# Kernel optimization log

Measured on AMD Instinct MI355X. Metric: run time of the kernel, lower is better.

The kernel has to match this reference:

```python
import jax, jax.numpy as jnp
import numpy as np
import math

RADIUS = 1.0
PERCENTAGES = (0.004, 0.006, 0.008, 0.01, 0.012)
REPULSION_H = 0.0005


def pairwise_sqdist(a, b):
    # a: [..., M, 3], b: [..., N, 3] -> [..., M, N] squared euclidean distances
    d = (jnp.sum(a * a, -1)[..., :, None] + jnp.sum(b * b, -1)[..., None, :]
         - 2.0 * jnp.einsum('...md,...nd->...mn', a, b))
    return jnp.maximum(d, 0.0)


def fps_indices(pts, npoint):
    # furthest point sampling for one cloud; pts [N,3] -> [npoint] int32 (starts at index 0)
    N = pts.shape[0]
    def body(carry, _):
        mind, last = carry
        d = jnp.sum((pts - pts[last]) ** 2, axis=-1)
        mind = jnp.minimum(mind, d)
        nxt = jnp.argmax(mind).astype(jnp.int32)
        return (mind, nxt), nxt
    init = (jnp.full((N,), 1e10, pts.dtype), jnp.int32(0))
    _, idxs = jax.lax.scan(body, init, None, length=npoint - 1)
    return jnp.concatenate([jnp.zeros((1,), jnp.int32), idxs])


def ball_query(pcd, new_xyz, r, nsample):
    # pcd [B,N,3], new_xyz [B,S,3] -> idx [B,S,nsample] int32
    # first-found-in-order semantics, pad with first valid index (pn2 ball_query)
    B, N, _ = pcd.shape
    sqd = pairwise_sqdist(new_xyz, pcd)                 # [B,S,N]
    mask = sqd < (r * r)
    key = jnp.where(mask, jnp.arange(N, dtype=jnp.int32)[None, None, :], jnp.int32(N))
    order = jnp.sort(key, axis=-1)[..., :nsample]       # in-ball indices first, ascending
    first = order[..., :1]                              # query is in cloud -> always valid
    return jnp.where(order == N, first, order)


def uniform_loss(pcd, radius=RADIUS):
    B, N, _ = pcd.shape
    npoint = int(N * 0.05)
    fps_idx = jax.vmap(fps_indices, in_axes=(0, None))(pcd, npoint)       # [B,npoint]
    new_xyz = jax.vmap(lambda p, i: p[i])(pcd, fps_idx)                    # [B,npoint,3]
    loss = jnp.float32(0.0)
    for p in PERCENTAGES:
        nsample = int(N * p)
        r = math.sqrt(p * radius)
        disk_area = math.pi * (radius ** 2) / N
        expect_len = math.sqrt(disk_area)
        idx = ball_query(pcd, new_xyz, r, nsample)                         # [B,npoint,nsample]
        grouped = jax.vmap(lambda pc, i: pc[i])(pcd, idx)                  # [B,npoint,nsample,3]
        g = grouped.reshape(B * npoint, nsample, 3)
        sqd = pairwise_sqdist(g, g)                                        # [G,ns,ns]
        # KNN k=2: two smallest sqdists; index 1 is nearest non-self neighbor
        sq2 = -jax.lax.top_k(-sqd, 2)[0][..., 1]                           # [G,ns]
        dist = jnp.sqrt(sq2 + 1e-12)                                       # knn returns euclidean dist
        uniform_dist = jnp.abs(dist + 1e-8)
        u = jnp.mean(uniform_dist, axis=1)                                 # [G]
        u = (u - expect_len) ** 2 / (expect_len + 1e-8)
        loss = loss + jnp.mean(u) * ((p * 100.0) ** 2)
    return loss / len(PERCENTAGES)


def repulsion_loss(pcd, h=REPULSION_H):
    sqd = pairwise_sqdist(pcd, pcd)                                        # [B,N,N]
    # knn k=20 then slice [:, :, 1:5]; only 5 smallest needed (same sorted values)
    vals = -jax.lax.top_k(-sqd, 5)[0]                                      # 5 smallest sqdists, ascending
    d = vals[..., 1:5]                                                     # dist**2 == sqdist
    return jnp.mean(jnp.maximum(h - d, 0.0))


def setup_inputs() -> dict:
    key = jax.random.key(0)
    pcd = jax.random.normal(key, (8, 4096, 3), dtype=jnp.float32)
    return {"pcd": pcd}


def reference(pcd):
    return uniform_loss(pcd) + repulsion_loss(pcd)
```

## Files before the change

### kernel.cpp

```cpp
#include <hip/hip_runtime.h>
#include <cmath>
#include <cstdint>

#define NB 8
#define NPTS 4096
#define NPOINT 204
#define NCENT (NB * NPOINT)

typedef unsigned long long u64;

struct BallParams { float thr[5]; int ns[5]; float el; float denom; };
struct FinalParams { double w[5]; };

template<int CTRL, int RMASK>
__device__ __forceinline__ u64 dpp_u64max_step(u64 v) {
    const int lo = (int)(unsigned)v, hi = (int)(unsigned)(v >> 32);
    const int lo2 = __builtin_amdgcn_update_dpp(lo, lo, CTRL, RMASK, 0xF, false);
    const int hi2 = __builtin_amdgcn_update_dpp(hi, hi, CTRL, RMASK, 0xF, false);
    const u64 o = ((u64)(unsigned)hi2 << 32) | (unsigned)lo2;
    return o > v ? o : v;
}
__device__ __forceinline__ u64 wave_u64max63(u64 v) {
    v = dpp_u64max_step<0x111, 0xF>(v);
    v = dpp_u64max_step<0x112, 0xF>(v);
    v = dpp_u64max_step<0x114, 0xF>(v);
    v = dpp_u64max_step<0x118, 0xF>(v);
    v = dpp_u64max_step<0x142, 0xA>(v);
    v = dpp_u64max_step<0x143, 0xC>(v);
    return v;
}
__device__ __forceinline__ u64 u64max(u64 a, u64 b) { return a > b ? a : b; }

__global__ __launch_bounds__(512) void fused_fps_rep(const float* __restrict__ pcd,
                                                     int* __restrict__ fps,
                                                     double* __restrict__ part)
{
#pragma clang fp contract(off)
    __shared__ float4 spts[NPTS];
    __shared__ int fps_lds[NPOINT];
    __shared__ __align__(16) u64 exch[2][8];
    __shared__ double wsum[8];

    const int t = threadIdx.x;
    const int lane = t & 63, wv = t >> 6;

    if (blockIdx.x < NB) {
        const int b = blockIdx.x;
        const float* base = pcd + (size_t)b * NPTS * 3;

        for (int j = t; j < NPTS; j += 512)
            spts[j] = make_float4(base[3*j], base[3*j+1], base[3*j+2], 0.f);

        const int pbase = t * 8;
        float px[8], py[8], pz[8], md[8];
#pragma unroll
        for (int k = 0; k < 8; ++k) {
            px[k] = base[(pbase + k) * 3 + 0];
            py[k] = base[(pbase + k) * 3 + 1];
            pz[k] = base[(pbase + k) * 3 + 2];
            md[k] = 1e10f;
        }
        if (t == 0) fps_lds[0] = 0;
        __syncthreads();

        float lx = spts[0].x, ly = spts[0].y, lz = spts[0].z;

        for (int it = 1; it < NPOINT; ++it) {
            u64 c[8];
#pragma unroll
            for (int k = 0; k < 8; ++k) {
                const float dx = px[k] - lx, dy = py[k] - ly, dz = pz[k] - lz;
                float d = dx * dx + dy * dy;
                d = d + dz * dz;
                const float m = fminf(md[k], d);
                md[k] = m;
                c[k] = ((u64)(unsigned)__float_as_int(m) << 32)
                     | (unsigned)(4095 - (pbase + k));
            }
#pragma unroll
            for (int s = 4; s >= 1; s >>= 1)
#pragma unroll
                for (int i = 0; i < 8; ++i)
                    if (i < s) c[i] = u64max(c[i], c[i + s]);
            const u64 wmax = wave_u64max63(c[0]);

            if (lane == 63) exch[it & 1][wv] = wmax;
            __syncthreads();

            const ulonglong2* e = (const ulonglong2*)&exch[it & 1][0];
            const ulonglong2 E0 = e[0], E1 = e[1], E2 = e[2], E3 = e[3];
            u64 m01 = u64max(E0.x, E0.y), m23 = u64max(E1.x, E1.y);
            u64 m45 = u64max(E2.x, E2.y), m67 = u64max(E3.x, E3.y);
            const u64 m = u64max(u64max(m01, m23), u64max(m45, m67));
            const int bi = 4095 - (int)((unsigned)m & 0xFFFu);

            if (t == 0) fps_lds[it] = bi;
            const float4 cc = spts[bi];
            lx = cc.x; ly = cc.y; lz = cc.z;
        }
        __syncthreads();
        for (int j = t; j < NPOINT; j += 512) fps[b * NPOINT + j] = fps_lds[j];
    } else {
        const int bb = blockIdx.x - NB;
        const int batch = bb >> 6;
        const int chunk = bb & 63;
        const float* base = pcd + (size_t)batch * NPTS * 3;

        for (int j = t; j < NPTS; j += 512) {
            const float x = base[j * 3 + 0], y = base[j * 3 + 1], z = base[j * 3 + 2];
            const float qs = (x * x + y * y) + z * z;
            spts[j] = make_float4(x, y, z, qs);
        }
        __syncthreads();

        const float h = 0.0005f;
        double acc = 0.0;

        for (int ii = 0; ii < 8; ++ii) {
            const int i = (chunk << 6) + (wv << 3) + ii;
            const float4 C = spts[i];
            const float cx = C.x, cy = C.y, cz = C.z, cs = C.w;
            float s0 = 3e38f, s1 = 3e38f, s2 = 3e38f, s3 = 3e38f;
            for (int bj = 0; bj < NPTS; bj += 64) {
                const int j = bj + lane;
                const float4 o = spts[j];
                const float dot = (cx * o.x + cy * o.y) + cz * o.z;
                const float d = fmaxf((cs + o.w) - 2.0f * dot, 0.0f);
                const bool q = (d < h) && (j != i);
                unsigned long long bal = __ballot(q);
                while (bal) {
                    const int src = __ffsll((unsigned long long)bal) - 1;
                    bal &= bal - 1;
                    const float dv = __shfl(d, src);
                    if (dv < s0) { s3 = s2; s2 = s1; s1 = s0; s0 = dv; }
                    else if (dv < s1) { s3 = s2; s2 = s1; s1 = dv; }
                    else if (dv < s2) { s3 = s2; s2 = dv; }
                    else if (dv < s3) { s3 = dv; }
                }
            }
            if (lane == 0) {
                if (s0 < h) acc += (double)(h - s0);
                if (s1 < h) acc += (double)(h - s1);
                if (s2 < h) acc += (double)(h - s2);
                if (s3 < h) acc += (double)(h - s3);
            }
        }
        if (lane == 0) wsum[wv] = acc;
        __syncthreads();
        if (t == 0) {
            double s = 0.0;
            for (int w = 0; w < 8; ++w) s += wsum[w];
            part[bb] = s;
        }
    }
}

__global__ __launch_bounds__(256) void ball_kernel(const float* __restrict__ pcd,
                                                   const int* __restrict__ fps,
                                                   double* __restrict__ uvals,
                                                   BallParams P)
{
#pragma clang fp contract(off)
    __shared__ float sqs[NPTS];
    __shared__ int wlist[4][5][52];
    __shared__ float4 gpts[4][64];

    const int wave = threadIdx.x >> 6;
    const int lane = threadIdx.x & 63;
    const int c = blockIdx.x * 4 + wave;
    const int b = c / NPOINT;
    const int m = c % NPOINT;

    const float* base = pcd + (size_t)b * NPTS * 3;
    for (int j = threadIdx.x; j < NPTS; j += 256) {
        const float x = base[j * 3 + 0], y = base[j * 3 + 1], z = base[j * 3 + 2];
        sqs[j] = (x * x + y * y) + z * z;
    }
    __syncthreads();

    const int ci = fps[b * NPOINT + m];
    const float cx = base[ci * 3 + 0], cy = base[ci * 3 + 1], cz = base[ci * 3 + 2];
    const float cs = sqs[ci];

    const int ns0 = P.ns[0], ns1 = P.ns[1], ns2 = P.ns[2], ns3 = P.ns[3], ns4 = P.ns[4];
    int cnt[5] = {0, 0, 0, 0, 0};
    const u64 lmask = (1ull << lane) - 1ull;

    for (int bj = 0; bj < NPTS; bj += 64) {
        const int j = bj + lane;
        const float qx = base[j * 3 + 0], qy = base[j * 3 + 1], qz = base[j * 3 + 2];
        const float qs = sqs[j];
        const float dot = (cx * qx + cy * qy) + cz * qz;
        const float d = fmaxf((cs + qs) - 2.0f * dot, 0.0f);

        const u64 bal4 = __ballot(d < P.thr[4]);
        if (bal4) {
#pragma unroll
            for (int p = 0; p < 4; ++p) {
                const bool q = d < P.thr[p];
                const u64 bal = __ballot(q);
                if (q) {
                    const int pos = cnt[p] + __popcll(bal & lmask);
                    if (pos < P.ns[p]) wlist[wave][p][pos] = j;
                }
                cnt[p] += __popcll(bal);
            }
            if (d < P.thr[4]) {
                const int pos = cnt[4] + __popcll(bal4 & lmask);
                if (pos < ns4) wlist[wave][4][pos] = j;
            }
            cnt[4] += __popcll(bal4);
            if (cnt[0] >= ns0 && cnt[1] >= ns1 && cnt[2] >= ns2 &&
                cnt[3] >= ns3 && cnt[4] >= ns4) break;
        }
    }

#pragma unroll
    for (int p = 0; p < 5; ++p) {
        const int nsample = P.ns[p];
        const int m_in = (cnt[p] < nsample) ? cnt[p] : nsample;
        const int gidx = wlist[wave][p][(lane < m_in) ? lane : 0];
        const float gx = base[gidx * 3 + 0], gy = base[gidx * 3 + 1], gz = base[gidx * 3 + 2];
        const float gs = sqs[gidx];
        gpts[wave][lane] = make_float4(gx, gy, gz, gs);

        float m1 = 3.0e38f, m2 = 3.0e38f;
        for (int j = 0; j < nsample; ++j) {
            const float4 o = gpts[wave][j];
            const float dot = (gx * o.x + gy * o.y) + gz * o.z;
            const float d = fmaxf((gs + o.w) - 2.0f * dot, 0.0f);
            if (d < m1) { m2 = m1; m1 = d; }
            else if (d < m2) { m2 = d; }
        }
        float ud = (lane < nsample) ? fabsf(sqrtf(m2 + 1e-12f) + 1e-8f) : 0.0f;
        for (int off = 32; off; off >>= 1) ud += __shfl_xor(ud, off);
        if (lane == 0) {
            const float um   = ud / (float)nsample;
            const float diff = um - P.el;
            const float u    = (diff * diff) / P.denom;
            uvals[p * NCENT + c] = (double)u;
        }
    }
}

__global__ __launch_bounds__(256) void final_kernel(const double* __restrict__ uvals,
                                                    const double* __restrict__ part,
                                                    float* __restrict__ out,
                                                    FinalParams F)
{
    __shared__ double red[6][4];
    const int t = threadIdx.x;
    const int lane = t & 63, wv = t >> 6;

    double s[6] = {0.0, 0.0, 0.0, 0.0, 0.0, 0.0};
    for (int c = t; c < NCENT; c += 256) {
        s[0] += uvals[0 * NCENT + c];
        s[1] += uvals[1 * NCENT + c];
        s[2] += uvals[2 * NCENT + c];
        s[3] += uvals[3 * NCENT + c];
        s[4] += uvals[4 * NCENT + c];
    }
    for (int c = t; c < NB * 64; c += 256) s[5] += part[c];

    for (int off = 32; off; off >>= 1) {
#pragma unroll
        for (int p = 0; p < 6; ++p) s[p] += __shfl_xor(s[p], off);
    }
    if (lane == 0) {
#pragma unroll
        for (int p = 0; p < 6; ++p) red[p][wv] = s[p];
    }
    __syncthreads();
    if (t == 0) {
        double sums[6];
#pragma unroll
        for (int p = 0; p < 6; ++p)
            sums[p] = ((red[p][0] + red[p][1]) + red[p][2]) + red[p][3];
        double loss = 0.0;
        loss += (sums[0] / (double)NCENT) * F.w[0];
        loss += (sums[1] / (double)NCENT) * F.w[1];
        loss += (sums[2] / (double)NCENT) * F.w[2];
        loss += (sums[3] / (double)NCENT) * F.w[3];
        loss += (sums[4] / (double)NCENT) * F.w[4];
        loss /= 5.0;
        const double rep = sums[5] / (double)(NB * NPTS * 4);
        out[0] = (float)(loss + rep);
    }
}

extern "C" void kernel_launch(void* const* d_in, const int* in_sizes, int n_in,
                              void* d_out, int out_size, void* d_ws, size_t ws_size,
                              hipStream_t stream)
{
    const float* pcd = (const float*)d_in[0];
    float* out = (float*)d_out;

    int*    fps   = (int*)d_ws;
    double* uvals = (double*)((char*)d_ws + 8192);
    double* repp  = (double*)((char*)d_ws + 8192 + (size_t)5 * NCENT * 8);

    const double pv[5] = {0.004, 0.006, 0.008, 0.01, 0.012};
    const int    nsv[5] = {16, 24, 32, 40, 49};

    BallParams bp;
    FinalParams fp;
    for (int i = 0; i < 5; ++i) {
        const double r = sqrt(pv[i]);
        bp.thr[i] = (float)(r * r);
        bp.ns[i]  = nsv[i];
        const double w = pv[i] * 100.0;
        fp.w[i] = w * w;
    }
    const double el = sqrt(3.141592653589793 / 4096.0);
    bp.el    = (float)el;
    bp.denom = (float)(el + 1e-8);

    fused_fps_rep<<<NB + NB * 64, 512, 0, stream>>>(pcd, fps, repp);
    ball_kernel<<<NCENT / 4, 256, 0, stream>>>(pcd, fps, uvals, bp);
    final_kernel<<<1, 256, 0, stream>>>(uvals, repp, out, fp);
}
```

Measured before the change: 175.4 us.

## Split each ball query across four waves and drop shared sqnorm table

Each block now handles one centroid instead of four. Its four waves each scan a quarter of the point cloud, and the per-wave in-ball lists are merged in order through shared counts. The five radius groups are then spread across the waves for the nearest-neighbour step. The per-block 4096-entry squared-norm table is replaced by computing norms inline. This shortens the serial scan per centroid and removes the shared-memory preload, but gives up the early-exit break, so all points are always scanned.

```diff
diff --git a/kernel.cpp b/kernel.cpp
--- a/kernel.cpp
+++ b/kernel.cpp
@@ -161,35 +161,29 @@
                                                    BallParams P)
 {
 #pragma clang fp contract(off)
-    __shared__ float sqs[NPTS];
     __shared__ int wlist[4][5][52];
+    __shared__ int scnt[4][5];
     __shared__ float4 gpts[4][64];
 
     const int wave = threadIdx.x >> 6;
     const int lane = threadIdx.x & 63;
-    const int c = blockIdx.x * 4 + wave;
+    const int c = blockIdx.x;
     const int b = c / NPOINT;
     const int m = c % NPOINT;
 
     const float* base = pcd + (size_t)b * NPTS * 3;
-    for (int j = threadIdx.x; j < NPTS; j += 256) {
-        const float x = base[j * 3 + 0], y = base[j * 3 + 1], z = base[j * 3 + 2];
-        sqs[j] = (x * x + y * y) + z * z;
-    }
-    __syncthreads();
-
     const int ci = fps[b * NPOINT + m];
     const float cx = base[ci * 3 + 0], cy = base[ci * 3 + 1], cz = base[ci * 3 + 2];
-    const float cs = sqs[ci];
-
-    const int ns0 = P.ns[0], ns1 = P.ns[1], ns2 = P.ns[2], ns3 = P.ns[3], ns4 = P.ns[4];
+    const float cs = (cx * cx + cy * cy) + cz * cz;
+
     int cnt[5] = {0, 0, 0, 0, 0};
     const u64 lmask = (1ull << lane) - 1ull;
 
-    for (int bj = 0; bj < NPTS; bj += 64) {
-        const int j = bj + lane;
+    const int j0 = wave << 10;
+    for (int bj = 0; bj < 1024; bj += 64) {
+        const int j = j0 + bj + lane;
         const float qx = base[j * 3 + 0], qy = base[j * 3 + 1], qz = base[j * 3 + 2];
-        const float qs = sqs[j];
+        const float qs = (qx * qx + qy * qy) + qz * qz;
         const float dot = (cx * qx + cy * qy) + cz * qz;
         const float d = fmaxf((cs + qs) - 2.0f * dot, 0.0f);
 
@@ -207,21 +201,36 @@
             }
             if (d < P.thr[4]) {
                 const int pos = cnt[4] + __popcll(bal4 & lmask);
-                if (pos < ns4) wlist[wave][4][pos] = j;
+                if (pos < P.ns[4]) wlist[wave][4][pos] = j;
             }
             cnt[4] += __popcll(bal4);
-            if (cnt[0] >= ns0 && cnt[1] >= ns1 && cnt[2] >= ns2 &&
-                cnt[3] >= ns3 && cnt[4] >= ns4) break;
-        }
-    }
-
-#pragma unroll
-    for (int p = 0; p < 5; ++p) {
+        }
+    }
+    if (lane == 0) {
+#pragma unroll
+        for (int p = 0; p < 5; ++p) scnt[wave][p] = cnt[p];
+    }
+    __syncthreads();
+
+    const int np_of[4]  = {1, 1, 1, 2};
+    const int p0_of[4]  = {4, 3, 2, 0};
+    for (int pi = 0; pi < np_of[wave]; ++pi) {
+        const int p = p0_of[wave] + pi;
         const int nsample = P.ns[p];
-        const int m_in = (cnt[p] < nsample) ? cnt[p] : nsample;
-        const int gidx = wlist[wave][p][(lane < m_in) ? lane : 0];
+        const int n0 = scnt[0][p], n1 = scnt[1][p], n2 = scnt[2][p], n3 = scnt[3][p];
+        const int total = ((n0 + n1) + n2) + n3;
+        const int m_in = (total < nsample) ? total : nsample;
+
+        auto src_of = [&](int pos) -> int {
+            int w = 0, q = pos;
+            if (q >= n0) { q -= n0; w = 1;
+                if (q >= n1) { q -= n1; w = 2;
+                    if (q >= n2) { q -= n2; w = 3; } } }
+            return wlist[w][p][q];
+        };
+        const int gidx = src_of((lane < m_in) ? lane : 0);
         const float gx = base[gidx * 3 + 0], gy = base[gidx * 3 + 1], gz = base[gidx * 3 + 2];
-        const float gs = sqs[gidx];
+        const float gs = (gx * gx + gy * gy) + gz * gz;
         gpts[wave][lane] = make_float4(gx, gy, gz, gs);
 
         float m1 = 3.0e38f, m2 = 3.0e38f;
@@ -316,6 +325,6 @@
     bp.denom = (float)(el + 1e-8);
 
     fused_fps_rep<<<NB + NB * 64, 512, 0, stream>>>(pcd, fps, repp);
-    ball_kernel<<<NCENT / 4, 256, 0, stream>>>(pcd, fps, uvals, bp);
+    ball_kernel<<<NCENT, 256, 0, stream>>>(pcd, fps, uvals, bp);
     final_kernel<<<1, 256, 0, stream>>>(uvals, repp, out, fp);
 }
```

After: 159.4 us. 9.1% less time.
